# Kernel tuning notes

Measured on AMD Instinct MI355X. Metric: run time of the kernel, lower is better.

The kernel has to match this reference:

```python
import jax, jax.numpy as jnp
import numpy as np

B, T, D, H, O = 8, 16384, 256, 256, 256


def setup_inputs() -> dict:
    key = jax.random.key(0)
    ks = jax.random.split(key, 7)
    lim_d = 1.0 / np.sqrt(D)
    lim_h = 1.0 / np.sqrt(H)
    u = lambda k, shape, lim: jax.random.uniform(k, shape, jnp.float32, -lim, lim)
    return {
        "xs": jax.random.normal(ks[0], (B, T, D), jnp.float32),
        "Wz": u(ks[1], (H, D), lim_d),
        "bz": u(ks[2], (H,), lim_d),
        "Wh": u(ks[3], (H, D), lim_d),
        "bh": u(ks[4], (H,), lim_d),
        "Wo": u(ks[5], (O, H), lim_h),
        "bo": u(ks[6], (O,), lim_h),
    }


def reference(xs, Wz, bz, Wh, bh, Wo, bo):
    # gates and candidate hidden states (eqx.nn.Linear: y = W @ x + b)
    zs = jax.nn.sigmoid(jnp.einsum("btd,hd->bth", xs, Wz) + bz)  # [B,T,H]
    hs = jnp.einsum("btd,hd->bth", xs, Wh) + bh                  # [B,T,H]

    # prepend_ones / prepend_zeros along the time axis
    a = jnp.concatenate([jnp.ones_like(zs[:, :1]), 1.0 - zs], axis=1)    # [B,T+1,H]
    b = jnp.concatenate([jnp.zeros_like(zs[:, :1]), zs * hs], axis=1)    # [B,T+1,H]

    def combine(first, second):
        a0, b0 = first
        a1, b1 = second
        return (a0 * b0, b0 * a1 + b1)

    _, states = jax.lax.associative_scan(combine, (a, b), axis=1)
    return jnp.einsum("bth,oh->bto", states[:, 1:], Wo) + bo  # [B,T,O]
```

## Files before the change

### kernel.cpp

```cpp
#include <hip/hip_runtime.h>
#include <hip/hip_bf16.h>

#define Bsz 8
#define Tsz 16384
#define NL0 16385
#define NL5 512
#define NL10 16

typedef __attribute__((ext_vector_type(2))) float f32x2;
typedef __attribute__((ext_vector_type(4))) float f32x4;
typedef __attribute__((ext_vector_type(8))) short bf16x8;

__device__ __forceinline__ short f2bf(float f) {
  unsigned u = __builtin_bit_cast(unsigned, f);
  u += 0x7FFFu + ((u >> 16) & 1u);
  return (short)(u >> 16);
}
__device__ __forceinline__ unsigned cvtpk(float lo, float hi) {
  __hip_bfloat162 t = __float22bfloat162_rn(float2{lo, hi});
  unsigned u;
  __builtin_memcpy(&u, &t, 4);
  return u;
}
__device__ __forceinline__ bf16x8 pack8(f32x4 a, f32x4 b) {
  union { unsigned u[4]; bf16x8 v; } r;
  r.u[0] = cvtpk(a[0], a[1]); r.u[1] = cvtpk(a[2], a[3]);
  r.u[2] = cvtpk(b[0], b[1]); r.u[3] = cvtpk(b[2], b[3]);
  return r.v;
}
__device__ __forceinline__ void unpk(unsigned u, float& a, float& b) {
  a = __builtin_bit_cast(float, u << 16);
  b = __builtin_bit_cast(float, u & 0xFFFF0000u);
}

__global__ void fill_sentinel(float* __restrict__ out, int n) {
  int i = blockIdx.x * blockDim.x + threadIdx.x;
  if (i < n) out[i] = 12345.0f;
}

__global__ void prep_weights(const float* __restrict__ Wz, const float* __restrict__ Wh,
                             const float* __restrict__ Wo, unsigned short* __restrict__ wt) {
  int idx = blockIdx.x * 256 + threadIdx.x;
  if (idx >= 3 * 256 * 32) return;
  int m   = idx >> 13;
  int rem = idx & 8191;
  int r   = rem >> 5;
  int cq  = rem & 31;
  const float* src = (m == 0 ? Wz : (m == 1 ? Wh : Wo)) + r * 256 + cq * 8;
  f32x4 v0 = *(const f32x4*)src;
  f32x4 v1 = *(const f32x4*)(src + 4);
  *(bf16x8*)(wt + m * 65536 + (cq * 256 + r) * 8) = pack8(v0, v1);
}

__global__ void init_e0(unsigned* __restrict__ l0) {
  int idx = blockIdx.x * 256 + threadIdx.x;
  if (idx >= Bsz * 256) return;
  int batch = idx >> 8, h = idx & 255;
  l0[(size_t)batch * NL0 * 256 + h] = 0x00003F80u;
}

__global__ __launch_bounds__(256, 3)
void gemm_zh(const float* __restrict__ xs, const unsigned short* __restrict__ wt,
             const float* __restrict__ bz, const float* __restrict__ bh,
             unsigned* __restrict__ l0)
{
  __shared__ __align__(16) unsigned short aL[32][32][8];

  const int tid = threadIdx.x;
  const int wave = tid >> 6, lane = tid & 63, l15 = lane & 15, l4 = lane >> 4;
  const int rowBase = blockIdx.x * 32;
  const float* base = xs + (size_t)rowBase * 256;
  const unsigned short* wz_t = wt;
  const unsigned short* wh_t = wt + 65536;
  const int wn = wave * 64;

  {
    f32x4 av0[4], av1[4];
#pragma unroll
    for (int k = 0; k < 4; ++k) {
      av0[k] = *(const f32x4*)(base + tid * 8 + k * 2048);
      av1[k] = *(const f32x4*)(base + tid * 8 + k * 2048 + 4);
    }
#pragma unroll
    for (int k = 0; k < 4; ++k) {
      const int o = tid + k * 256;
      const int row = o >> 5, oct = o & 31;
      *(bf16x8*)&aL[row][oct ^ (row & 7)][0] = pack8(av0[k], av1[k]);
    }
  }
  __syncthreads();

  f32x4 accz[2][4] = {};
  f32x4 acch[2][4] = {};

#pragma unroll
  for (int kk = 0; kk < 8; ++kk) {
    bf16x8 af[2];
#pragma unroll
    for (int m = 0; m < 2; ++m) {
      const int row = m * 16 + l15;
      af[m] = *(const bf16x8*)&aL[row][(kk * 4 + l4) ^ (row & 7)][0];
    }
    const int cq = kk * 4 + l4;
    bf16x8 zf[4], hf[4];
#pragma unroll
    for (int n = 0; n < 4; ++n) {
      const int r = wn + n * 16 + l15;
      zf[n] = *(const bf16x8*)(wz_t + (cq * 256 + r) * 8);
      hf[n] = *(const bf16x8*)(wh_t + (cq * 256 + r) * 8);
    }
#pragma unroll
    for (int m = 0; m < 2; ++m)
#pragma unroll
      for (int n = 0; n < 4; ++n) {
        accz[m][n] = __builtin_amdgcn_mfma_f32_16x16x32_bf16(af[m], zf[n], accz[m][n], 0, 0, 0);
        acch[m][n] = __builtin_amdgcn_mfma_f32_16x16x32_bf16(af[m], hf[n], acch[m][n], 0, 0, 0);
      }
  }

  const int batch = rowBase >> 14;
  const int tRow  = rowBase & (Tsz - 1);
#pragma unroll
  for (int n = 0; n < 4; ++n) {
    const int col = wn + n * 16 + l15;
    const float bzv = bz[col], bhv = bh[col];
#pragma unroll
    for (int m = 0; m < 2; ++m)
#pragma unroll
      for (int j = 0; j < 4; ++j) {
        const int t = tRow + m * 16 + l4 * 4 + j;
        const float zv = 1.0f / (1.0f + __expf(-(accz[m][n][j] + bzv)));
        const float hv = acch[m][n][j] + bhv;
        l0[((size_t)batch * NL0 + t + 1) * 256 + col] = cvtpk(1.0f - zv, zv * hv);
      }
  }
}

__global__ __launch_bounds__(256)
void chunk_up_bf16(const unsigned* __restrict__ l0, f32x2* __restrict__ dst)
{
  int idx = blockIdx.x * 256 + threadIdx.x;
  int h2 = idx & 127, r = idx >> 7;
  int c = r & 511, batch = r >> 9;
  size_t base = ((size_t)batch * NL0 + (size_t)c * 32) * 256 + h2 * 2;

  float ax[16], bx[16], ay[16], by[16];
#pragma unroll
  for (int i = 0; i < 16; ++i) {
    uint2 e0 = *(const uint2*)(l0 + base + (size_t)(2 * i) * 256);
    uint2 e1 = *(const uint2*)(l0 + base + (size_t)(2 * i + 1) * 256);
    float a0, b0, a1, b1;
    unpk(e0.x, a0, b0); unpk(e1.x, a1, b1);
    ax[i] = a0 * b0; bx[i] = b0 * a1 + b1;
    unpk(e0.y, a0, b0); unpk(e1.y, a1, b1);
    ay[i] = a0 * b0; by[i] = b0 * a1 + b1;
  }
#pragma unroll
  for (int n = 8; n >= 1; n >>= 1) {
#pragma unroll
    for (int i = 0; i < n; ++i) {
      float nax = ax[2*i] * bx[2*i], nbx = bx[2*i] * ax[2*i+1] + bx[2*i+1];
      float nay = ay[2*i] * by[2*i], nby = by[2*i] * ay[2*i+1] + by[2*i+1];
      ax[i] = nax; bx[i] = nbx; ay[i] = nay; by[i] = nby;
    }
  }
  f32x4 o = {ax[0], bx[0], ay[0], by[0]};
  *(f32x4*)((float*)dst + (((size_t)batch * 512 + c) * 256 + h2 * 2) * 2) = o;
}

__global__ __launch_bounds__(256)
void chunk_up(const f32x2* __restrict__ src, f32x2* __restrict__ dst, int nCh, int nSrc)
{
  int idx = blockIdx.x * 256 + threadIdx.x;
  int total = Bsz * nCh * 256;
  if (idx >= total) return;
  int h = idx & 255, r = idx >> 8;
  int c = r % nCh, batch = r / nCh;
  size_t base = ((size_t)batch * nSrc + (size_t)c * 32) * 256 + h;

  float a1[16], b1[16];
#pragma unroll
  for (int i = 0; i < 16; ++i) {
    f32x2 e0 = src[base + (size_t)(2 * i) * 256];
    f32x2 e1 = src[base + (size_t)(2 * i + 1) * 256];
    a1[i] = e0[0] * e0[1];
    b1[i] = e0[1] * e1[0] + e1[1];
  }
#pragma unroll
  for (int n = 8; n >= 1; n >>= 1) {
#pragma unroll
    for (int i = 0; i < n; ++i) {
      float na = a1[2 * i] * b1[2 * i];
      float nb = b1[2 * i] * a1[2 * i + 1] + b1[2 * i + 1];
      a1[i] = na; b1[i] = nb;
    }
  }
  dst[((size_t)batch * nCh + c) * 256 + h] = f32x2{a1[0], b1[0]};
}

__global__ void tree16(const f32x2* __restrict__ src, float* __restrict__ outB)
{
  int idx = blockIdx.x * 256 + threadIdx.x;
  if (idx >= Bsz * 256) return;
  int h = idx & 255, batch = idx >> 8;
  size_t base = (size_t)batch * 16 * 256 + h;

  float a0[16], b0[16];
#pragma unroll
  for (int i = 0; i < 16; ++i) { f32x2 e = src[base + (size_t)i * 256]; a0[i] = e[0]; b0[i] = e[1]; }
  float a1[8], b1[8];
#pragma unroll
  for (int i = 0; i < 8; ++i) { a1[i] = a0[2*i]*b0[2*i]; b1[i] = b0[2*i]*a0[2*i+1] + b0[2*i+1]; }
  float a2[4], b2[4];
#pragma unroll
  for (int i = 0; i < 4; ++i) { a2[i] = a1[2*i]*b1[2*i]; b2[i] = b1[2*i]*a1[2*i+1] + b1[2*i+1]; }
  float a3[2], b3[2];
#pragma unroll
  for (int i = 0; i < 2; ++i) { a3[i] = a2[2*i]*b2[2*i]; b3[i] = b2[2*i]*a2[2*i+1] + b2[2*i+1]; }
  float s3[2];
  s3[0] = b3[0];
  s3[1] = b3[0] * a3[1] + b3[1];
  float s2[4];
  s2[0] = b2[0]; s2[1] = s3[0]; s2[2] = s3[0] * a2[2] + b2[2]; s2[3] = s3[1];
  float s1[8];
  s1[0] = b1[0];
#pragma unroll
  for (int j = 0; j < 4; ++j) s1[2*j+1] = s2[j];
#pragma unroll
  for (int j = 1; j < 4; ++j) s1[2*j] = s2[j-1] * a1[2*j] + b1[2*j];
  float s0[16];
  s0[0] = b0[0];
#pragma unroll
  for (int j = 0; j < 8; ++j) s0[2*j+1] = s1[j];
#pragma unroll
  for (int j = 1; j < 8; ++j) s0[2*j] = s1[j-1] * a0[2*j] + b0[2*j];
#pragma unroll
  for (int i = 0; i < 16; ++i) outB[base + (size_t)i * 256] = s0[i];
}

__global__ __launch_bounds__(256, 2)
void chunk_down_f32(const f32x2* __restrict__ src, const float* __restrict__ snext,
                    float* __restrict__ outF, int nCh, int nFull, int nSrc)
{
  int idx = blockIdx.x * 256 + threadIdx.x;
  int total = Bsz * nCh * 256;
  if (idx >= total) return;
  int h = idx & 255, r = idx >> 8;
  int c = r % nCh, batch = r / nCh;
  size_t base = ((size_t)batch * nSrc + (size_t)c * 32) * 256 + h;
  bool hasP = (c > 0);
  float P = hasP ? snext[((size_t)batch * nFull + (c - 1)) * 256 + h] : 0.0f;
  float S = snext[((size_t)batch * nFull + c) * 256 + h];

  float ae[16], be[16], a1[16], b1[16];
#pragma unroll
  for (int i = 0; i < 16; ++i) {
    f32x2 e0 = src[base + (size_t)(2 * i) * 256];
    f32x2 e1 = src[base + (size_t)(2 * i + 1) * 256];
    ae[i] = e0[0]; be[i] = e0[1];
    a1[i] = e0[0] * e0[1];
    b1[i] = e0[1] * e1[0] + e1[1];
  }
  float a2[8], b2[8];
#pragma unroll
  for (int i = 0; i < 8; ++i) { a2[i] = a1[2*i]*b1[2*i]; b2[i] = b1[2*i]*a1[2*i+1] + b1[2*i+1]; }
  float a3[4], b3[4];
#pragma unroll
  for (int i = 0; i < 4; ++i) { a3[i] = a2[2*i]*b2[2*i]; b3[i] = b2[2*i]*a2[2*i+1] + b2[2*i+1]; }
  float a4[2], b4[2];
#pragma unroll
  for (int i = 0; i < 2; ++i) { a4[i] = a3[2*i]*b3[2*i]; b4[i] = b3[2*i]*a3[2*i+1] + b3[2*i+1]; }

  float s4[2];
  s4[0] = hasP ? P * a4[0] + b4[0] : b4[0];
  s4[1] = S;
  float s3[4];
  s3[0] = hasP ? P * a3[0] + b3[0] : b3[0];
  s3[1] = s4[0]; s3[2] = s4[0] * a3[2] + b3[2]; s3[3] = s4[1];
  float s2[8];
  s2[0] = hasP ? P * a2[0] + b2[0] : b2[0];
#pragma unroll
  for (int j = 0; j < 4; ++j) s2[2*j+1] = s3[j];
#pragma unroll
  for (int j = 1; j < 4; ++j) s2[2*j] = s3[j-1] * a2[2*j] + b2[2*j];
  float s1[16];
  s1[0] = hasP ? P * a1[0] + b1[0] : b1[0];
#pragma unroll
  for (int j = 0; j < 8; ++j) s1[2*j+1] = s2[j];
#pragma unroll
  for (int j = 1; j < 8; ++j) s1[2*j] = s2[j-1] * a1[2*j] + b1[2*j];

  outF[base] = hasP ? P * ae[0] + be[0] : be[0];
#pragma unroll
  for (int j = 0; j < 16; ++j) outF[base + (size_t)(2*j+1) * 256] = s1[j];
#pragma unroll
  for (int j = 1; j < 16; ++j) outF[base + (size_t)(2*j) * 256] = s1[j-1] * ae[j] + be[j];
}

__global__ __launch_bounds__(256, 2)
void down_proj(const unsigned* __restrict__ l0, const float* __restrict__ s5b,
               const unsigned short* __restrict__ wo_t, const float* __restrict__ bo,
               float* __restrict__ out)
{
  __shared__ unsigned short pL[32 * 256];

  const int tid = threadIdx.x;
  const int bc = blockIdx.x;
  const int c = bc % 513;
  const int batch = bc / 513;

  {
    const int h = tid;
    const size_t base = ((size_t)batch * NL0 + (size_t)c * 32) * 256 + h;
    const bool hasP = (c > 0);
    const float P = hasP ? s5b[((size_t)batch * 512 + (c - 1)) * 256 + h] : 0.0f;

    if (c == 512) {
      float a0, b0; unpk(l0[base], a0, b0);
      pL[h] = (unsigned short)f2bf(P * a0 + b0);
#pragma unroll
      for (int i = 1; i < 32; ++i)
        pL[i * 256 + (h ^ ((i & 7) << 3))] = 0;
    } else {
      const float S = s5b[((size_t)batch * 512 + c) * 256 + h];
      float ae[16], be[16], a1[16], b1[16];
#pragma unroll
      for (int i = 0; i < 16; ++i) {
        unsigned u0 = l0[base + (size_t)(2 * i) * 256];
        unsigned u1 = l0[base + (size_t)(2 * i + 1) * 256];
        float a0, b0, a1e, b1e;
        unpk(u0, a0, b0); unpk(u1, a1e, b1e);
        ae[i] = a0; be[i] = b0;
        a1[i] = a0 * b0; b1[i] = b0 * a1e + b1e;
      }
      float a2[8], b2[8];
#pragma unroll
      for (int i = 0; i < 8; ++i) { a2[i] = a1[2*i]*b1[2*i]; b2[i] = b1[2*i]*a1[2*i+1] + b1[2*i+1]; }
      float a3[4], b3[4];
#pragma unroll
      for (int i = 0; i < 4; ++i) { a3[i] = a2[2*i]*b2[2*i]; b3[i] = b2[2*i]*a2[2*i+1] + b2[2*i+1]; }
      float a4[2], b4[2];
#pragma unroll
      for (int i = 0; i < 2; ++i) { a4[i] = a3[2*i]*b3[2*i]; b4[i] = b3[2*i]*a3[2*i+1] + b3[2*i+1]; }

      float s4[2];
      s4[0] = hasP ? P * a4[0] + b4[0] : b4[0];
      s4[1] = S;
      float s3[4];
      s3[0] = hasP ? P * a3[0] + b3[0] : b3[0];
      s3[1] = s4[0]; s3[2] = s4[0] * a3[2] + b3[2]; s3[3] = s4[1];
      float s2[8];
      s2[0] = hasP ? P * a2[0] + b2[0] : b2[0];
#pragma unroll
      for (int j = 0; j < 4; ++j) s2[2*j+1] = s3[j];
#pragma unroll
      for (int j = 1; j < 4; ++j) s2[2*j] = s3[j-1] * a2[2*j] + b2[2*j];
      float s1[16];
      s1[0] = hasP ? P * a1[0] + b1[0] : b1[0];
#pragma unroll
      for (int j = 0; j < 8; ++j) s1[2*j+1] = s2[j];
#pragma unroll
      for (int j = 1; j < 8; ++j) s1[2*j] = s2[j-1] * a1[2*j] + b1[2*j];

      pL[h] = (unsigned short)f2bf(hasP ? P * ae[0] + be[0] : be[0]);
#pragma unroll
      for (int j = 0; j < 16; ++j) {
        const int row = 2 * j + 1;
        pL[row * 256 + (h ^ ((row & 7) << 3))] = (unsigned short)f2bf(s1[j]);
      }
#pragma unroll
      for (int j = 1; j < 16; ++j) {
        const int row = 2 * j;
        pL[row * 256 + (h ^ ((row & 7) << 3))] = (unsigned short)f2bf(s1[j-1] * ae[j] + be[j]);
      }
    }
  }
  __syncthreads();

  const int wave = tid >> 6, lane = tid & 63, l15 = lane & 15, l4 = lane >> 4;
  const int wn = wave * 64;
  f32x4 acc[2][4] = {};
  bf16x8 wc[4], wnx[4];
#pragma unroll
  for (int n = 0; n < 4; ++n)
    wc[n] = *(const bf16x8*)(wo_t + (l4 * 256 + wn + n * 16 + l15) * 8);
#pragma unroll
  for (int kk = 0; kk < 8; ++kk) {
    if (kk < 7) {
#pragma unroll
      for (int n = 0; n < 4; ++n)
        wnx[n] = *(const bf16x8*)(wo_t + (((kk + 1) * 4 + l4) * 256 + wn + n * 16 + l15) * 8);
    }
    bf16x8 af[2];
#pragma unroll
    for (int m = 0; m < 2; ++m) {
      const int row = m * 16 + l15;
      af[m] = *(const bf16x8*)&pL[row * 256 + ((kk * 32 + l4 * 8) ^ ((row & 7) << 3))];
    }
#pragma unroll
    for (int m = 0; m < 2; ++m)
#pragma unroll
      for (int n = 0; n < 4; ++n)
        acc[m][n] = __builtin_amdgcn_mfma_f32_16x16x32_bf16(af[m], wc[n], acc[m][n], 0, 0, 0);
    if (kk < 7) {
      wc[0] = wnx[0]; wc[1] = wnx[1]; wc[2] = wnx[2]; wc[3] = wnx[3];
    }
  }

  const int tBase = 32 * c - 1;
#pragma unroll
  for (int n = 0; n < 4; ++n) {
    const int col = wn + n * 16 + l15;
    const float bv = bo[col];
#pragma unroll
    for (int m = 0; m < 2; ++m)
#pragma unroll
      for (int j = 0; j < 4; ++j) {
        const int t = tBase + m * 16 + l4 * 4 + j;
        if ((unsigned)t < (unsigned)Tsz)
          out[((size_t)batch * Tsz + t) * 256 + col] = acc[m][n][j] + bv;
      }
  }
}

extern "C" void kernel_launch(void* const* d_in, const int* in_sizes, int n_in,
                              void* d_out, int out_size, void* d_ws, size_t ws_size,
                              hipStream_t stream)
{
  (void)in_sizes; (void)n_in;
  const float* xs = (const float*)d_in[0];
  const float* Wz = (const float*)d_in[1];
  const float* bz = (const float*)d_in[2];
  const float* Wh = (const float*)d_in[3];
  const float* bh = (const float*)d_in[4];
  const float* Wo = (const float*)d_in[5];
  const float* bo = (const float*)d_in[6];
  float* out = (float*)d_out;

  const size_t n_l0  = (size_t)Bsz * NL0 * 256;
  const size_t n_l5  = (size_t)Bsz * NL5 * 256;
  const size_t n_l10 = (size_t)Bsz * NL10 * 256;

  unsigned* l0    = (unsigned*)d_ws;
  f32x2* l5ab     = (f32x2*)(l0 + n_l0);
  f32x2* l10ab    = l5ab + n_l5;
  float* s10b     = (float*)(l10ab + n_l10);
  float* s5b      = s10b + n_l10;
  unsigned short* wt = (unsigned short*)(s5b + n_l5);

  const size_t need = n_l0 * 4 + n_l5 * 8 + n_l10 * 8 + n_l10 * 4 + n_l5 * 4 + 3 * 65536 * 2;
  if (ws_size < need) {
    fill_sentinel<<<(out_size + 255) / 256, 256, 0, stream>>>(out, out_size);
    return;
  }

  prep_weights<<<96, 256, 0, stream>>>(Wz, Wh, Wo, wt);
  init_e0<<<8, 256, 0, stream>>>(l0);
  gemm_zh<<<Bsz * Tsz / 32, 256, 0, stream>>>(xs, wt, bz, bh, l0);

  chunk_up_bf16<<<(Bsz * 512 * 128) / 256, 256, 0, stream>>>(l0, l5ab);
  chunk_up<<<(Bsz * 16 * 256) / 256, 256, 0, stream>>>(l5ab, l10ab, 16, NL5);
  tree16<<<8, 256, 0, stream>>>(l10ab, s10b);
  chunk_down_f32<<<(Bsz * 16 * 256) / 256, 256, 0, stream>>>(l5ab, s10b, s5b, 16, 16, NL5);

  down_proj<<<Bsz * 513, 256, 0, stream>>>(l0, s5b, wt + 2 * 65536, bo, out);
}
```

Before: 181.9 us.

## Fuse first-level chunk scan into gate GEMM epilogue and drop init kernel

The gate/candidate GEMM now computes tiles aligned to the scan's 32-element chunks (shifted by one row so the prepended identity element lands in chunk 0). It reduces each chunk in registers with cross-lane shuffles and writes the level-5 (a,b) summary directly. This removes the separate chunk_up_bf16 pass, which re-read the whole bf16 l0 buffer, and the init_e0 launch. The cost is a slightly larger grid (513 blocks per batch with clamped, misaligned row loads) and extra epilogue arithmetic and shuffles in the GEMM.

```diff
diff --git a/kernel.cpp b/kernel.cpp
--- a/kernel.cpp
+++ b/kernel.cpp
@@ -52,24 +52,19 @@
   *(bf16x8*)(wt + m * 65536 + (cq * 256 + r) * 8) = pack8(v0, v1);
 }
 
-__global__ void init_e0(unsigned* __restrict__ l0) {
-  int idx = blockIdx.x * 256 + threadIdx.x;
-  if (idx >= Bsz * 256) return;
-  int batch = idx >> 8, h = idx & 255;
-  l0[(size_t)batch * NL0 * 256 + h] = 0x00003F80u;
-}
-
 __global__ __launch_bounds__(256, 3)
 void gemm_zh(const float* __restrict__ xs, const unsigned short* __restrict__ wt,
              const float* __restrict__ bz, const float* __restrict__ bh,
-             unsigned* __restrict__ l0)
+             unsigned* __restrict__ l0, f32x2* __restrict__ l5)
 {
   __shared__ __align__(16) unsigned short aL[32][32][8];
 
   const int tid = threadIdx.x;
   const int wave = tid >> 6, lane = tid & 63, l15 = lane & 15, l4 = lane >> 4;
-  const int rowBase = blockIdx.x * 32;
-  const float* base = xs + (size_t)rowBase * 256;
+  const int bid = blockIdx.x;
+  const int batch = bid / 513;
+  const int cb = bid - batch * 513;
+  const long gr0 = (long)batch * Tsz + 32L * cb - 1;
   const unsigned short* wz_t = wt;
   const unsigned short* wh_t = wt + 65536;
   const int wn = wave * 64;
@@ -78,8 +73,13 @@
     f32x4 av0[4], av1[4];
 #pragma unroll
     for (int k = 0; k < 4; ++k) {
-      av0[k] = *(const f32x4*)(base + tid * 8 + k * 2048);
-      av1[k] = *(const f32x4*)(base + tid * 8 + k * 2048 + 4);
+      const int row = (tid >> 5) + k * 8;
+      const int col = (tid & 31) * 8;
+      long gr = gr0 + row;
+      gr = gr < 0 ? 0 : (gr > (long)Bsz * Tsz - 1 ? (long)Bsz * Tsz - 1 : gr);
+      const float* p = xs + gr * 256 + col;
+      av0[k] = *(const f32x4*)p;
+      av1[k] = *(const f32x4*)(p + 4);
     }
 #pragma unroll
     for (int k = 0; k < 4; ++k) {
@@ -118,8 +118,7 @@
       }
   }
 
-  const int batch = rowBase >> 14;
-  const int tRow  = rowBase & (Tsz - 1);
+  const int idx0 = 32 * cb;
 #pragma unroll
   for (int n = 0; n < 4; ++n) {
     const int col = wn + n * 16 + l15;
@@ -128,44 +127,48 @@
     for (int m = 0; m < 2; ++m)
 #pragma unroll
       for (int j = 0; j < 4; ++j) {
-        const int t = tRow + m * 16 + l4 * 4 + j;
+        const int e = m * 16 + l4 * 4 + j;
         const float zv = 1.0f / (1.0f + __expf(-(accz[m][n][j] + bzv)));
         const float hv = acch[m][n][j] + bhv;
-        l0[((size_t)batch * NL0 + t + 1) * 256 + col] = cvtpk(1.0f - zv, zv * hv);
-      }
-  }
-}
-
-__global__ __launch_bounds__(256)
-void chunk_up_bf16(const unsigned* __restrict__ l0, f32x2* __restrict__ dst)
-{
-  int idx = blockIdx.x * 256 + threadIdx.x;
-  int h2 = idx & 127, r = idx >> 7;
-  int c = r & 511, batch = r >> 9;
-  size_t base = ((size_t)batch * NL0 + (size_t)c * 32) * 256 + h2 * 2;
-
-  float ax[16], bx[16], ay[16], by[16];
-#pragma unroll
-  for (int i = 0; i < 16; ++i) {
-    uint2 e0 = *(const uint2*)(l0 + base + (size_t)(2 * i) * 256);
-    uint2 e1 = *(const uint2*)(l0 + base + (size_t)(2 * i + 1) * 256);
-    float a0, b0, a1, b1;
-    unpk(e0.x, a0, b0); unpk(e1.x, a1, b1);
-    ax[i] = a0 * b0; bx[i] = b0 * a1 + b1;
-    unpk(e0.y, a0, b0); unpk(e1.y, a1, b1);
-    ay[i] = a0 * b0; by[i] = b0 * a1 + b1;
-  }
-#pragma unroll
-  for (int n = 8; n >= 1; n >>= 1) {
-#pragma unroll
-    for (int i = 0; i < n; ++i) {
-      float nax = ax[2*i] * bx[2*i], nbx = bx[2*i] * ax[2*i+1] + bx[2*i+1];
-      float nay = ay[2*i] * by[2*i], nby = by[2*i] * ay[2*i+1] + by[2*i+1];
-      ax[i] = nax; bx[i] = nbx; ay[i] = nay; by[i] = nby;
-    }
-  }
-  f32x4 o = {ax[0], bx[0], ay[0], by[0]};
-  *(f32x4*)((float*)dst + (((size_t)batch * 512 + c) * 256 + h2 * 2) * 2) = o;
+        float a = 1.0f - zv, b = zv * hv;
+        if (cb == 0 && e == 0) { a = 1.0f; b = 0.0f; }
+        const unsigned u = cvtpk(a, b);
+        if (cb < 512 || e == 0)
+          l0[((size_t)batch * NL0 + idx0 + e) * 256 + col] = u;
+        float ar, br; unpk(u, ar, br);
+        accz[m][n][j] = ar; acch[m][n][j] = br;
+      }
+  }
+
+  if (cb < 512) {
+    const bool f3 = (l4 & 1) == 0;
+    const bool f4 = (l4 & 2) == 0;
+#pragma unroll
+    for (int n = 0; n < 4; ++n) {
+      float a4v[2], b4v[2];
+#pragma unroll
+      for (int m = 0; m < 2; ++m) {
+        const float a10 = accz[m][n][0] * acch[m][n][0];
+        const float b10 = acch[m][n][0] * accz[m][n][1] + acch[m][n][1];
+        const float a11 = accz[m][n][2] * acch[m][n][2];
+        const float b11 = acch[m][n][2] * accz[m][n][3] + acch[m][n][3];
+        const float a2 = a10 * b10;
+        const float b2 = b10 * a11 + b11;
+        const float pa = __shfl_xor(a2, 16);
+        const float pb = __shfl_xor(b2, 16);
+        const float a3 = f3 ? a2 * b2 : pa * pb;
+        const float b3 = f3 ? b2 * pa + pb : pb * a2 + b2;
+        const float qa = __shfl_xor(a3, 32);
+        const float qb = __shfl_xor(b3, 32);
+        a4v[m] = f4 ? a3 * b3 : qa * qb;
+        b4v[m] = f4 ? b3 * qa + qb : qb * a3 + b3;
+      }
+      const float a5 = a4v[0] * b4v[0];
+      const float b5 = b4v[0] * a4v[1] + b4v[1];
+      if (l4 == 0)
+        l5[((size_t)batch * 512 + cb) * 256 + wn + n * 16 + l15] = f32x2{a5, b5};
+    }
+  }
 }
 
 __global__ __launch_bounds__(256)
@@ -455,10 +458,8 @@
   }
 
   prep_weights<<<96, 256, 0, stream>>>(Wz, Wh, Wo, wt);
-  init_e0<<<8, 256, 0, stream>>>(l0);
-  gemm_zh<<<Bsz * Tsz / 32, 256, 0, stream>>>(xs, wt, bz, bh, l0);
-
-  chunk_up_bf16<<<(Bsz * 512 * 128) / 256, 256, 0, stream>>>(l0, l5ab);
+  gemm_zh<<<Bsz * 513, 256, 0, stream>>>(xs, wt, bz, bh, l0, l5ab);
+
   chunk_up<<<(Bsz * 16 * 256) / 256, 256, 0, stream>>>(l5ab, l10ab, 16, NL5);
   tree16<<<8, 256, 0, stream>>>(l10ab, s10b);
   chunk_down_f32<<<(Bsz * 16 * 256) / 256, 256, 0, stream>>>(l5ab, s10b, s5b, 16, 16, NL5);
```

After: 171.6 us. 5.7% less time.
